# Performance work log

Hardware: AMD Instinct MI355X
Metric: run time of the kernel (lower is better)

## Reference

```python
import jax, jax.numpy as jnp
import numpy as np

B, S, L, D = 4, 8, 350, 768  # paragraphs, sentences/paragraph, padded pair length, hidden
P = B * S * (S - 1)          # number of ordered sentence pairs = 224

# pair p -> (z, j, k): same enumeration order as the torch nested loops
_IDX = np.array([(z, j, k) for z in range(B) for j in range(S) for k in range(S) if j != k])
# each pair contributes its first-sentence embedding to segment (z,j) and second to (z,k)
_SEG = np.stack([_IDX[:, 0] * S + _IDX[:, 1], _IDX[:, 0] * S + _IDX[:, 2]], axis=1).reshape(-1)  # [2P]


def setup_inputs() -> dict:
    key = jax.random.key(0)
    ks = jax.random.split(key, 8)
    sc = 0.02
    all_output = jax.random.normal(ks[0], (P, L, D), dtype=jnp.float32)
    first_sep = jax.random.randint(ks[1], (P,), 5, 150).astype(jnp.int32)           # > 1
    second_sep = (first_sep + jax.random.randint(ks[2], (P,), 5, 150)).astype(jnp.int32)  # > first_sep+1, < L
    W1 = jax.random.normal(ks[3], (D, D), dtype=jnp.float32) * sc
    b1 = jnp.zeros((D,), jnp.float32)
    v1 = jax.random.normal(ks[4], (D,), dtype=jnp.float32) * sc
    vb1 = jnp.zeros((), jnp.float32)
    W2 = jax.random.normal(ks[5], (D, D), dtype=jnp.float32) * sc
    b2 = jnp.zeros((D,), jnp.float32)
    v2 = jax.random.normal(ks[6], (D,), dtype=jnp.float32) * sc
    vb2 = jnp.zeros((), jnp.float32)
    return {"all_output": all_output, "first_sep": first_sep, "second_sep": second_sep,
            "W1": W1, "b1": b1, "v1": v1, "vb1": vb1,
            "W2": W2, "b2": b2, "v2": v2, "vb2": vb2}


def reference(all_output, first_sep, second_sep, W1, b1, v1, vb1, W2, b2, v2, vb2):
    # pair_embeddings = [CLS] token of every pair
    pair_embeddings = all_output[:, 0, :]  # [P, D]

    # ---- level one: masked attention pooling over word positions ----
    u = jnp.tanh(all_output @ W1 + b1)          # [P, L, D]
    scores = u @ v1 + vb1                       # [P, L]
    pos = jnp.arange(L)[None, :]                # [1, L]
    mask1 = (pos >= 1) & (pos < first_sep[:, None])                 # tokens 1..first_sep-1
    mask2 = (pos > first_sep[:, None]) & (pos < second_sep[:, None])  # first_sep+1..second_sep-1

    def pool(mask):
        s = jnp.where(mask, scores, -jnp.inf)
        w = jax.nn.softmax(s, axis=1)           # [P, L]
        return jnp.einsum('pl,pld->pd', w, all_output)

    e1 = pool(mask1)                            # [P, D] first-sentence embeddings
    e2 = pool(mask2)                            # [P, D] second-sentence embeddings
    emb = jnp.stack([e1, e2], axis=1).reshape(2 * P, D)  # [2P, D]

    # ---- level two: segment attention pooling per (paragraph, sentence) group ----
    seg = jnp.asarray(_SEG)                     # [2P] segment ids, num_segments = B*S
    u2 = jnp.tanh(emb @ W2 + b2)                # [2P, D]
    sc = u2 @ v2 + vb2                          # [2P]
    num_seg = B * S
    smax = jax.ops.segment_max(sc, seg, num_segments=num_seg)
    ex = jnp.exp(sc - smax[seg])
    denom = jax.ops.segment_sum(ex, seg, num_segments=num_seg)
    w = ex / denom[seg]                         # segment softmax weights
    out2 = jax.ops.segment_sum(w[:, None] * emb, seg, num_segments=num_seg).reshape(B, S, D)
    return (pair_embeddings, out2)
```

## Files before the change

kernel.cpp:

```cpp
#include <hip/hip_runtime.h>
#include <math.h>

#define LSEQ   350
#define DDIM   768
#define NPAIR  224
#define MROWS1 78400
#define NSLAB1 613
#define MAXSLAB 520
#define SPROWS 66688

typedef short bf16x8 __attribute__((ext_vector_type(8)));
typedef float f32x4  __attribute__((ext_vector_type(4)));

typedef const unsigned int __attribute__((address_space(1)))* gas_ptr;
typedef unsigned int __attribute__((address_space(3)))* las_ptr;

__device__ __forceinline__ void gload_lds16(const void* g, void* l) {
  __builtin_amdgcn_global_load_lds((gas_ptr)g, (las_ptr)l, 16, 0, 0);
}

__device__ __forceinline__ unsigned short f2bf(float x) {
  unsigned int u = __float_as_uint(x);
  unsigned int r = (u + 0x7FFFu + ((u >> 16) & 1u)) >> 16;
  return (unsigned short)r;
}

__device__ __forceinline__ float tanh_fast(float x) {
  float e = __expf(2.f * x);
  return 1.f - 2.f / (e + 1.f);
}

#define PREP_CV 2688
#define PREP_WT 1152
#define PREP_ZB 337
#define PREP_SCAN (PREP_CV + PREP_WT)
__global__ __launch_bounds__(256) void k_prep(
    const float* __restrict__ X, const float* __restrict__ W1,
    const float* __restrict__ W2, unsigned short* __restrict__ Wt1,
    unsigned short* __restrict__ Wt2, const int* __restrict__ ssep,
    int* __restrict__ off, unsigned int* __restrict__ zreg,
    unsigned short* __restrict__ Xbf) {
  const int b = blockIdx.x;
  const int t = threadIdx.x;
  if (b < PREP_CV) {
    const int p = b / 12;
    const int rem = b - p * 12;
    const int nrow = ssep[p] - 1;
    const int r0 = (rem >> 2) * 128 + (rem & 3) * 32;
    if (r0 >= nrow) return;
    const int lane = t & 63;
    int accv = 0;
    for (int i = lane; i < NPAIR; i += 64) accv += (i < p) ? (ssep[i] - 1) : 0;
#pragma unroll
    for (int d = 1; d < 64; d <<= 1) accv += __shfl_xor(accv, d);
    const int o = accv;
    if (t < 192) {
      const int half = t / 96;
      const int tt = t - half * 96;
      const int rmax = min(32, nrow - r0);
      const float* src = X + ((size_t)p * LSEQ + 1 + r0) * DDIM + tt * 8;
      unsigned short* dst = Xbf + (size_t)(o + r0) * DDIM + tt * 8;
#pragma unroll 4
      for (int rr = half; rr < rmax; rr += 2) {
        const float* s = src + (size_t)rr * DDIM;
        float4 x = *(const float4*)s;
        float4 y = *(const float4*)(s + 4);
        unsigned int ux = __float_as_uint(x.x) + 0x8000u;
        unsigned int uy = __float_as_uint(x.y) + 0x8000u;
        unsigned int uz = __float_as_uint(x.z) + 0x8000u;
        unsigned int uw = __float_as_uint(x.w) + 0x8000u;
        unsigned int vx = __float_as_uint(y.x) + 0x8000u;
        unsigned int vy = __float_as_uint(y.y) + 0x8000u;
        unsigned int vz = __float_as_uint(y.z) + 0x8000u;
        unsigned int vw = __float_as_uint(y.w) + 0x8000u;
        *(uint4*)(dst + (size_t)rr * DDIM) =
            make_uint4(__builtin_amdgcn_perm(uy, ux, 0x07060302u),
                       __builtin_amdgcn_perm(uw, uz, 0x07060302u),
                       __builtin_amdgcn_perm(vy, vx, 0x07060302u),
                       __builtin_amdgcn_perm(vw, vz, 0x07060302u));
      }
    }
  } else if (b < PREP_SCAN) {
    const int br = b - PREP_CV;
    const float* W = (br >= 576) ? W2 : W1;
    unsigned short* Wt = (br >= 576) ? Wt2 : Wt1;
    const int r = (br >= 576) ? br - 576 : br;
    const int bk = (r % 24) * 32, bn = (r / 24) * 32;
    __shared__ float tile[32][33];
    const int tx = t & 31, ty = t >> 5;
#pragma unroll
    for (int i = 0; i < 32; i += 8)
      tile[ty + i][tx] = W[(size_t)(bk + ty + i) * DDIM + bn + tx];
    __syncthreads();
#pragma unroll
    for (int i = 0; i < 32; i += 8)
      Wt[(size_t)(bn + ty + i) * DDIM + bk + tx] = f2bf(tile[tx][ty + i]);
  } else if (b == PREP_SCAN) {
    __shared__ int buf[256];
    int v = (t < NPAIR) ? (ssep[t] - 1) : 0;
    buf[t] = v;
    __syncthreads();
#pragma unroll
    for (int d = 1; d < 256; d <<= 1) {
      int add = (t >= d) ? buf[t - d] : 0;
      __syncthreads();
      buf[t] += add;
      __syncthreads();
    }
    if (t < NPAIR) off[t] = buf[t] - v;
    if (t == NPAIR - 1) off[NPAIR] = buf[t];
  } else {
    const int i = b - PREP_SCAN - 1;
    *((uint4*)zreg + (size_t)i * 256 + t) = make_uint4(0u, 0u, 0u, 0u);
  }
}

__global__ __launch_bounds__(256, 4) void k_gemm_c(
    const unsigned short* __restrict__ Xbf, const unsigned short* __restrict__ Wt,
    const float* __restrict__ bias, const float* __restrict__ vv,
    const int* __restrict__ off, float* __restrict__ scores_part) {
  const int Mtotal = off[NPAIR];
  const int b = blockIdx.x;
  const int g = b / 48, r = b - g * 48;
  const int slab = g * 8 + (r & 7);
  const int nchunk = r >> 3;
  if (slab * 128 >= Mtotal) return;

  const size_t arow0 = (size_t)slab * 128;
  const int n0 = nchunk * 128;

  __shared__ unsigned short As[2][128 * 32];
  __shared__ unsigned short Bs[2][128 * 32];

  const int t = threadIdx.x;
  const int lane = t & 63, w = t >> 6;
  const int l15 = t & 15;
  const int quad = (t >> 4) & 3;
  const int wm = w >> 1, wn = w & 1;
  const int lrow = lane >> 2;
  const int scol = ((lane & 3) ^ ((lane >> 3) & 3)) * 8;

  f32x4 acc[4][4];
#pragma unroll
  for (int mi = 0; mi < 4; ++mi)
#pragma unroll
    for (int ni = 0; ni < 4; ++ni)
#pragma unroll
      for (int q = 0; q < 4; ++q) acc[mi][ni][q] = 0.f;

  auto stage = [&](int bi, int kk0) {
#pragma unroll
    for (int j = 0; j < 2; ++j) {
      int seg = w * 2 + j;
      gload_lds16(Xbf + (arow0 + seg * 16 + lrow) * DDIM + kk0 + scol, &As[bi][seg * 512]);
      gload_lds16(Wt + (size_t)(n0 + seg * 16 + lrow) * DDIM + kk0 + scol, &Bs[bi][seg * 512]);
    }
  };

  stage(0, 0);
  __syncthreads();

  const int qs = (quad ^ ((l15 >> 1) & 3)) * 8;
  int cur = 0;
#pragma unroll 1
  for (int step = 0; step < DDIM / 32; ++step) {
    if (step < DDIM / 32 - 1) stage(cur ^ 1, (step + 1) * 32);

    bf16x8 a[4], bfr[4];
#pragma unroll
    for (int mi = 0; mi < 4; ++mi)
      a[mi] = *(const bf16x8*)&As[cur][(wm * 64 + mi * 16 + l15) * 32 + qs];
#pragma unroll
    for (int ni = 0; ni < 4; ++ni)
      bfr[ni] = *(const bf16x8*)&Bs[cur][(wn * 64 + ni * 16 + l15) * 32 + qs];
#pragma unroll
    for (int mi = 0; mi < 4; ++mi)
#pragma unroll
      for (int ni = 0; ni < 4; ++ni)
        acc[mi][ni] = __builtin_amdgcn_mfma_f32_16x16x32_bf16(a[mi], bfr[ni], acc[mi][ni], 0, 0, 0);
    __syncthreads();
    cur ^= 1;
  }

  float vvv[4], bbv[4];
#pragma unroll
  for (int ni = 0; ni < 4; ++ni) {
    int n = n0 + wn * 64 + ni * 16 + l15;
    vvv[ni] = vv[n];
    bbv[ni] = bias[n];
  }
  float* spdst = scores_part + (size_t)(nchunk * 2 + wn) * SPROWS;
#pragma unroll
  for (int mi = 0; mi < 4; ++mi) {
#pragma unroll
    for (int reg = 0; reg < 4; ++reg) {
      float s = 0.f;
#pragma unroll
      for (int ni = 0; ni < 4; ++ni)
        s += tanh_fast(acc[mi][ni][reg] + bbv[ni]) * vvv[ni];
      s += __shfl_xor(s, 1);
      s += __shfl_xor(s, 2);
      s += __shfl_xor(s, 4);
      s += __shfl_xor(s, 8);
      if (l15 == mi * 4 + reg) {
        int row = (int)arow0 + wm * 64 + mi * 16 + quad * 4 + reg;
        if (row < Mtotal) spdst[row] = s;
      }
    }
  }
}

__global__ __launch_bounds__(256, 2) void k_gemm_score(
    const float* __restrict__ X, const unsigned short* __restrict__ Wt,
    const float* __restrict__ bias, const float* __restrict__ vv,
    float* __restrict__ outs, int Mrows, int swz) {
  int slab, nchunk;
  if (swz) {
    int b = blockIdx.x;
    int g = b / 48, r = b - g * 48;
    slab = g * 8 + (r & 7);
    nchunk = r >> 3;
    if (slab >= NSLAB1) return;
  } else {
    slab = blockIdx.y;
    nchunk = blockIdx.x;
  }
  const int row0 = slab * 128;
  const int n0 = nchunk * 128;

  __shared__ unsigned short As[128][40];
  __shared__ unsigned short Bs[128][40];

  const int t = threadIdx.x;
  const int l15 = t & 15;
  const int quad = (t >> 4) & 3;
  const int w = t >> 6;
  const int wm = w >> 1, wn = w & 1;
  const int ar = t >> 3;
  const int ac = (t & 7) * 4;
  const int br = t >> 2;
  const int bc = (t & 3) * 8;

  f32x4 acc[4][4];
#pragma unroll
  for (int mi = 0; mi < 4; ++mi)
#pragma unroll
    for (int ni = 0; ni < 4; ++ni)
#pragma unroll
      for (int q = 0; q < 4; ++q) acc[mi][ni][q] = 0.f;

  for (int k0 = 0; k0 < DDIM; k0 += 32) {
#pragma unroll
    for (int pass = 0; pass < 4; ++pass) {
      int rr = ar + pass * 32;
      int row = row0 + rr;
      float4 x = make_float4(0.f, 0.f, 0.f, 0.f);
      if (row < Mrows) x = *(const float4*)(X + (size_t)row * DDIM + k0 + ac);
      unsigned int ux = __float_as_uint(x.x) + 0x8000u;
      unsigned int uy = __float_as_uint(x.y) + 0x8000u;
      unsigned int uz = __float_as_uint(x.z) + 0x8000u;
      unsigned int uw = __float_as_uint(x.w) + 0x8000u;
      *(uint2*)&As[rr][ac] = make_uint2(__builtin_amdgcn_perm(uy, ux, 0x07060302u),
                                        __builtin_amdgcn_perm(uw, uz, 0x07060302u));
    }
#pragma unroll
    for (int pp = 0; pp < 2; ++pp) {
      int rr = br + pp * 64;
      *(uint4*)&Bs[rr][bc] = *(const uint4*)(Wt + (size_t)(n0 + rr) * DDIM + k0 + bc);
    }
    __syncthreads();

    bf16x8 a[4], bfr[4];
#pragma unroll
    for (int mi = 0; mi < 4; ++mi)
      a[mi] = *(const bf16x8*)&As[wm * 64 + mi * 16 + l15][quad * 8];
#pragma unroll
    for (int ni = 0; ni < 4; ++ni)
      bfr[ni] = *(const bf16x8*)&Bs[wn * 64 + ni * 16 + l15][quad * 8];
#pragma unroll
    for (int mi = 0; mi < 4; ++mi)
#pragma unroll
      for (int ni = 0; ni < 4; ++ni)
        acc[mi][ni] = __builtin_amdgcn_mfma_f32_16x16x32_bf16(a[mi], bfr[ni], acc[mi][ni], 0, 0, 0);
    __syncthreads();
  }

  float vvv[4], bbv[4];
#pragma unroll
  for (int ni = 0; ni < 4; ++ni) {
    int n = n0 + wn * 64 + ni * 16 + l15;
    vvv[ni] = vv[n];
    bbv[ni] = bias[n];
  }
#pragma unroll
  for (int mi = 0; mi < 4; ++mi) {
#pragma unroll
    for (int reg = 0; reg < 4; ++reg) {
      float s = 0.f;
#pragma unroll
      for (int ni = 0; ni < 4; ++ni)
        s += tanh_fast(acc[mi][ni][reg] + bbv[ni]) * vvv[ni];
      s += __shfl_xor(s, 1);
      s += __shfl_xor(s, 2);
      s += __shfl_xor(s, 4);
      s += __shfl_xor(s, 8);
      if (l15 == mi * 4 + reg) {
        int row = row0 + wm * 64 + mi * 16 + quad * 4 + reg;
        if (row < Mrows) atomicAdd(&outs[row], s);
      }
    }
  }
}

__device__ __forceinline__ float block_reduce(float v, bool is_max, float* redbuf) {
#pragma unroll
  for (int off = 1; off < 64; off <<= 1) {
    float o = __shfl_xor(v, off);
    v = is_max ? fmaxf(v, o) : (v + o);
  }
  int wv = threadIdx.x >> 6;
  if ((threadIdx.x & 63) == 0) redbuf[wv] = v;
  __syncthreads();
  float r = is_max ? fmaxf(fmaxf(redbuf[0], redbuf[1]), fmaxf(redbuf[2], redbuf[3]))
                   : (redbuf[0] + redbuf[1] + redbuf[2] + redbuf[3]);
  __syncthreads();
  return r;
}

__global__ __launch_bounds__(256) void k_pool3(
    const unsigned short* __restrict__ Xbf, const float* __restrict__ X,
    const float* __restrict__ sp, const int* __restrict__ fsep,
    const int* __restrict__ ssep, const int* __restrict__ off,
    float* __restrict__ emb, float* __restrict__ out) {
  const int p = blockIdx.x, c = blockIdx.y, t = threadIdx.x;
  const int fs = fsep[p], ss = ssep[p];
  const int o = off[p];
  __shared__ float sw1[LSEQ], sw2[LSEQ];
  __shared__ float redbuf[4];

  float m1p = -INFINITY, m2p = -INFINITY;
  for (int l = t; l < LSEQ; l += 256) {
    float s = 0.f;
    if (l >= 1 && l < ss) {
      const int idx = o + l - 1;
#pragma unroll
      for (int c6 = 0; c6 < 12; ++c6) s += sp[(size_t)c6 * SPROWS + idx];
    }
    float s1 = (l >= 1 && l < fs) ? s : -INFINITY;
    float s2 = (l > fs && l < ss) ? s : -INFINITY;
    sw1[l] = s1; sw2[l] = s2;
    m1p = fmaxf(m1p, s1); m2p = fmaxf(m2p, s2);
  }
  __syncthreads();
  float m1 = block_reduce(m1p, true, redbuf);
  float m2 = block_reduce(m2p, true, redbuf);
  float d1p = 0.f, d2p = 0.f;
  for (int l = t; l < LSEQ; l += 256) {
    float e1v = __expf(sw1[l] - m1);
    float e2v = __expf(sw2[l] - m2);
    sw1[l] = e1v; sw2[l] = e2v;
    d1p += e1v; d2p += e2v;
  }
  __syncthreads();
  float inv1 = 1.f / block_reduce(d1p, false, redbuf);
  float inv2 = 1.f / block_reduce(d2p, false, redbuf);

  if (t < 192) {
    if (c == 0) {
      *(float4*)(out + (size_t)p * DDIM + t * 4) =
          *(const float4*)(X + (size_t)p * LSEQ * DDIM + t * 4);
    }

    const int nch = (ss + 2) >> 2;
    const int lo = 1 + c * nch;
    const int hi = min(ss, lo + nch);

    float A1[4] = {0.f, 0.f, 0.f, 0.f}, A2[4] = {0.f, 0.f, 0.f, 0.f};
    const unsigned short* xb = Xbf + (size_t)o * DDIM + t * 4;
#pragma unroll 4
    for (int l = lo; l < hi; ++l) {
      float wa = sw1[l] * inv1, wb = sw2[l] * inv2;
      uint2 xv = *(const uint2*)(xb + (size_t)(l - 1) * DDIM);
      float x0 = __uint_as_float((xv.x & 0xFFFFu) << 16);
      float x1 = __uint_as_float(xv.x & 0xFFFF0000u);
      float x2 = __uint_as_float((xv.y & 0xFFFFu) << 16);
      float x3 = __uint_as_float(xv.y & 0xFFFF0000u);
      A1[0] += wa * x0; A1[1] += wa * x1; A1[2] += wa * x2; A1[3] += wa * x3;
      A2[0] += wb * x0; A2[1] += wb * x1; A2[2] += wb * x2; A2[3] += wb * x3;
    }
    float* e1 = emb + (size_t)(2 * p) * DDIM + t * 4;
    float* e2 = emb + (size_t)(2 * p + 1) * DDIM + t * 4;
    atomicAdd(&e1[0], A1[0]); atomicAdd(&e1[1], A1[1]);
    atomicAdd(&e1[2], A1[2]); atomicAdd(&e1[3], A1[3]);
    atomicAdd(&e2[0], A2[0]); atomicAdd(&e2[1], A2[1]);
    atomicAdd(&e2[2], A2[2]); atomicAdd(&e2[3], A2[3]);
  }
}

__global__ __launch_bounds__(256) void k_w1t(const float* __restrict__ W,
                                             unsigned short* __restrict__ Wt) {
  __shared__ float tile[32][33];
  int bk = blockIdx.x * 32, bn = blockIdx.y * 32;
  int tx = threadIdx.x & 31, ty = threadIdx.x >> 5;
#pragma unroll
  for (int i = 0; i < 32; i += 8)
    tile[ty + i][tx] = W[(size_t)(bk + ty + i) * DDIM + bn + tx];
  __syncthreads();
#pragma unroll
  for (int i = 0; i < 32; i += 8)
    Wt[(size_t)(bn + ty + i) * DDIM + bk + tx] = f2bf(tile[tx][ty + i]);
}

__global__ __launch_bounds__(256) void k_pool(
    const float* __restrict__ X, const float* __restrict__ scores,
    const int* __restrict__ fsep, const int* __restrict__ ssep,
    float* __restrict__ emb, float* __restrict__ out) {
  const int p = blockIdx.x;
  const int c = blockIdx.y;
  const int t = threadIdx.x;
  const int fs = fsep[p], ss = ssep[p];
  __shared__ float sw1[LSEQ], sw2[LSEQ];
  __shared__ float redbuf[4];

  float m1p = -INFINITY, m2p = -INFINITY;
  for (int l = t; l < LSEQ; l += 256) {
    float s = scores[p * LSEQ + l];
    float s1 = (l >= 1 && l < fs) ? s : -INFINITY;
    float s2 = (l > fs && l < ss) ? s : -INFINITY;
    sw1[l] = s1; sw2[l] = s2;
    m1p = fmaxf(m1p, s1); m2p = fmaxf(m2p, s2);
  }
  __syncthreads();
  float m1 = block_reduce(m1p, true, redbuf);
  float m2 = block_reduce(m2p, true, redbuf);
  float d1p = 0.f, d2p = 0.f;
  for (int l = t; l < LSEQ; l += 256) {
    float e1v = __expf(sw1[l] - m1);
    float e2v = __expf(sw2[l] - m2);
    sw1[l] = e1v; sw2[l] = e2v;
    d1p += e1v; d2p += e2v;
  }
  __syncthreads();
  float inv1 = 1.f / block_reduce(d1p, false, redbuf);
  float inv2 = 1.f / block_reduce(d2p, false, redbuf);
  const float* base = X + (size_t)p * LSEQ * DDIM;
  if (c == 0) {
    float* po = out + (size_t)p * DDIM;
    po[t] = base[t]; po[t + 256] = base[t + 256]; po[t + 512] = base[t + 512];
  }
  if (t < 192) {
    float4 A1 = make_float4(0.f, 0.f, 0.f, 0.f);
    float4 A2 = make_float4(0.f, 0.f, 0.f, 0.f);
    for (int l = 1 + c; l < ss; l += 8) {
      float wa = sw1[l] * inv1, wb = sw2[l] * inv2;
      float4 x = *(const float4*)(base + (size_t)l * DDIM + 4 * t);
      A1.x += wa * x.x; A1.y += wa * x.y; A1.z += wa * x.z; A1.w += wa * x.w;
      A2.x += wb * x.x; A2.y += wb * x.y; A2.z += wb * x.z; A2.w += wb * x.w;
    }
    float* e1 = emb + (size_t)(2 * p) * DDIM + 4 * t;
    float* e2 = emb + (size_t)(2 * p + 1) * DDIM + 4 * t;
    atomicAdd(&e1[0], A1.x); atomicAdd(&e1[1], A1.y);
    atomicAdd(&e1[2], A1.z); atomicAdd(&e1[3], A1.w);
    atomicAdd(&e2[0], A2.x); atomicAdd(&e2[1], A2.y);
    atomicAdd(&e2[2], A2.z); atomicAdd(&e2[3], A2.w);
  }
}

__global__ __launch_bounds__(256) void k_segout(
    const float* __restrict__ emb, const float* __restrict__ sc,
    float* __restrict__ out2) {
  const int g = blockIdx.x;
  const int z = g >> 3, j = g & 7;
  const int t = threadIdx.x;
  int ee[14];
#pragma unroll
  for (int i = 0; i < 7; ++i) ee[i] = 2 * (z * 56 + j * 7 + i);
#pragma unroll
  for (int i = 0; i < 7; ++i) {
    int j2 = i + (i >= j ? 1 : 0);
    int kk = j - (j > j2 ? 1 : 0);
    ee[7 + i] = 2 * (z * 56 + j2 * 7 + kk) + 1;
  }
  float sv[14];
  float m = -INFINITY;
#pragma unroll
  for (int i = 0; i < 14; ++i) { sv[i] = sc[ee[i]]; m = fmaxf(m, sv[i]); }
  float den = 0.f;
#pragma unroll
  for (int i = 0; i < 14; ++i) { sv[i] = __expf(sv[i] - m); den += sv[i]; }
  float inv = 1.f / den;
  float a0 = 0.f, a1 = 0.f, a2 = 0.f;
#pragma unroll
  for (int i = 0; i < 14; ++i) {
    float wgt = sv[i] * inv;
    const float* er = emb + (size_t)ee[i] * DDIM;
    a0 += wgt * er[t]; a1 += wgt * er[t + 256]; a2 += wgt * er[t + 512];
  }
  out2[(size_t)g * DDIM + t] = a0;
  out2[(size_t)g * DDIM + t + 256] = a1;
  out2[(size_t)g * DDIM + t + 512] = a2;
}

extern "C" void kernel_launch(void* const* d_in, const int* in_sizes, int n_in,
                              void* d_out, int out_size, void* d_ws, size_t ws_size,
                              hipStream_t stream) {
  const float* X  = (const float*)d_in[0];
  const int* fs   = (const int*)d_in[1];
  const int* ss   = (const int*)d_in[2];
  const float* W1 = (const float*)d_in[3];
  const float* b1 = (const float*)d_in[4];
  const float* v1 = (const float*)d_in[5];
  const float* W2 = (const float*)d_in[7];
  const float* b2 = (const float*)d_in[8];
  const float* v2 = (const float*)d_in[9];
  float* out = (float*)d_out;

  char* ws = (char*)d_ws;
  const size_t XBF_ROWS = (size_t)MAXSLAB * 128 + 128;
  const size_t OFF_OFF  = XBF_ROWS * DDIM * 2;
  const size_t OFF_WT1  = OFF_OFF + 1024;
  const size_t OFF_WT2  = OFF_WT1 + 1179648;
  const size_t OFF_SP   = OFF_WT2 + 1179648;
  const size_t OFF_SC2  = OFF_SP + (size_t)12 * SPROWS * 4;
  const size_t OFF_EMB  = OFF_SC2 + 2048;
  const size_t ZBYTES   = (size_t)PREP_ZB * 4096;
  const size_t NEED     = OFF_SC2 + ZBYTES + 256;

  if (ws_size >= NEED) {
    unsigned short* Xbf = (unsigned short*)ws;
    int*   off     = (int*)(ws + OFF_OFF);
    unsigned short* Wt1 = (unsigned short*)(ws + OFF_WT1);
    unsigned short* Wt2 = (unsigned short*)(ws + OFF_WT2);
    float* spart    = (float*)(ws + OFF_SP);
    float* sc       = (float*)(ws + OFF_SC2);
    float* emb      = (float*)(ws + OFF_EMB);

    k_prep<<<PREP_SCAN + 1 + PREP_ZB, 256, 0, stream>>>(
        X, W1, W2, Wt1, Wt2, ss, off, (unsigned int*)sc, Xbf);
    k_gemm_c<<<65 * 48, 256, 0, stream>>>(Xbf, Wt1, b1, v1, off, spart);
    k_pool3<<<dim3(NPAIR, 4), 256, 0, stream>>>(Xbf, X, spart, fs, ss, off, emb, out);
    k_gemm_score<<<dim3(6, 4), 256, 0, stream>>>(emb, Wt2, b2, v2, sc, 448, 0);
    k_segout<<<32, 256, 0, stream>>>(emb, sc, out + (size_t)NPAIR * DDIM);
  } else {
    unsigned short* Wt = (unsigned short*)ws;
    float* scores = (float*)(ws + 1179648);
    float* emb    = (float*)(ws + 1493248);
    float* sc     = scores;

    k_w1t<<<dim3(24, 24), 256, 0, stream>>>(W1, Wt);
    hipMemsetAsync(scores, 0, MROWS1 * sizeof(float), stream);
    hipMemsetAsync(emb, 0, 448 * DDIM * sizeof(float), stream);
    k_gemm_score<<<77 * 48, 256, 0, stream>>>(X, Wt, b1, v1, scores, MROWS1, 1);
    k_pool<<<dim3(NPAIR, 8), 256, 0, stream>>>(X, scores, fs, ss, emb, out);
    k_w1t<<<dim3(24, 24), 256, 0, stream>>>(W2, Wt);
    hipMemsetAsync(sc, 0, 448 * sizeof(float), stream);
    k_gemm_score<<<dim3(6, 4), 256, 0, stream>>>(emb, Wt, b2, v2, sc, 448, 0);
    k_segout<<<32, 256, 0, stream>>>(emb, sc, out + (size_t)NPAIR * DDIM);
  }
}
```

Baseline: 468.2 us.

## Enlarge compacted GEMM tile to 256x256x64 with 512 threads and interleaved staging

```diff
diff --git a/kernel.cpp b/kernel.cpp
--- a/kernel.cpp
+++ b/kernel.cpp
@@ -7,6 +7,7 @@
 #define MROWS1 78400
 #define NSLAB1 613
 #define MAXSLAB 520
+#define MAXSLAB256 260
 #define SPROWS 66688
 
 typedef short bf16x8 __attribute__((ext_vector_type(8)));
@@ -115,71 +116,89 @@
   }
 }
 
-__global__ __launch_bounds__(256, 4) void k_gemm_c(
+__global__ __launch_bounds__(512, 2) void k_gemm_c(
     const unsigned short* __restrict__ Xbf, const unsigned short* __restrict__ Wt,
     const float* __restrict__ bias, const float* __restrict__ vv,
     const int* __restrict__ off, float* __restrict__ scores_part) {
   const int Mtotal = off[NPAIR];
   const int b = blockIdx.x;
-  const int g = b / 48, r = b - g * 48;
+  const int g = b / 24, r = b - g * 24;
   const int slab = g * 8 + (r & 7);
   const int nchunk = r >> 3;
-  if (slab * 128 >= Mtotal) return;
-
-  const size_t arow0 = (size_t)slab * 128;
-  const int n0 = nchunk * 128;
-
-  __shared__ unsigned short As[2][128 * 32];
-  __shared__ unsigned short Bs[2][128 * 32];
+  if (slab * 256 >= Mtotal) return;
+
+  const size_t arow0 = (size_t)slab * 256;
+  const int n0 = nchunk * 256;
+
+  __shared__ unsigned short As[2][256 * 64];
+  __shared__ unsigned short Bs[2][256 * 64];
 
   const int t = threadIdx.x;
   const int lane = t & 63, w = t >> 6;
   const int l15 = t & 15;
   const int quad = (t >> 4) & 3;
-  const int wm = w >> 1, wn = w & 1;
-  const int lrow = lane >> 2;
-  const int scol = ((lane & 3) ^ ((lane >> 3) & 3)) * 8;
-
-  f32x4 acc[4][4];
-#pragma unroll
-  for (int mi = 0; mi < 4; ++mi)
+  const int wm = w >> 2, wn = w & 3;
+  const int srow = (lane >> 3);
+  const int scol = ((lane & 7) ^ ((lane >> 3) & 7)) * 8;
+
+  f32x4 acc[8][4];
+#pragma unroll
+  for (int mi = 0; mi < 8; ++mi)
 #pragma unroll
     for (int ni = 0; ni < 4; ++ni)
 #pragma unroll
       for (int q = 0; q < 4; ++q) acc[mi][ni][q] = 0.f;
 
-  auto stage = [&](int bi, int kk0) {
+  auto stage_half = [&](int bi, int kt, int h) {
+    unsigned short* lb = (h < 2 ? &As[bi][0] : &Bs[bi][0]) + (h & 1) * 128 * 64;
+    const unsigned short* gb = (h < 2)
+        ? Xbf + (arow0 + (h & 1) * 128) * (size_t)DDIM
+        : Wt + (size_t)(n0 + (h & 1) * 128) * DDIM;
 #pragma unroll
     for (int j = 0; j < 2; ++j) {
-      int seg = w * 2 + j;
-      gload_lds16(Xbf + (arow0 + seg * 16 + lrow) * DDIM + kk0 + scol, &As[bi][seg * 512]);
-      gload_lds16(Wt + (size_t)(n0 + seg * 16 + lrow) * DDIM + kk0 + scol, &Bs[bi][seg * 512]);
+      int strip = w * 2 + j;
+      int rr = strip * 8 + srow;
+      gload_lds16(gb + (size_t)rr * DDIM + kt * 64 + scol, lb + strip * 512);
     }
   };
 
-  stage(0, 0);
-  __syncthreads();
-
-  const int qs = (quad ^ ((l15 >> 1) & 3)) * 8;
-  int cur = 0;
+  auto compute_tile = [&](int rb, int sb, int kts) {
+    bf16x8 a[4], bb[4];
+    const int sw = l15 & 7;
+#pragma unroll
+    for (int half = 0; half < 2; ++half) {
+#pragma unroll
+      for (int ni = 0; ni < 4; ++ni)
+        bb[ni] = *(const bf16x8*)&Bs[rb][(wn * 64 + ni * 16 + l15) * 64 +
+                                         (((half << 2) + quad) ^ sw) * 8];
+#pragma unroll
+      for (int mg = 0; mg < 2; ++mg) {
+#pragma unroll
+        for (int mi = 0; mi < 4; ++mi)
+          a[mi] = *(const bf16x8*)&As[rb][(wm * 128 + (mg * 4 + mi) * 16 + l15) * 64 +
+                                          (((half << 2) + quad) ^ sw) * 8];
+        if (kts >= 0) stage_half(sb, kts, half * 2 + mg);
+#pragma unroll
+        for (int mi = 0; mi < 4; ++mi)
+#pragma unroll
+          for (int ni = 0; ni < 4; ++ni)
+            acc[mg * 4 + mi][ni] = __builtin_amdgcn_mfma_f32_16x16x32_bf16(
+                a[mi], bb[ni], acc[mg * 4 + mi][ni], 0, 0, 0);
+      }
+    }
+  };
+
+#pragma unroll
+  for (int h = 0; h < 4; ++h) stage_half(0, 0, h);
+  __syncthreads();
+
 #pragma unroll 1
-  for (int step = 0; step < DDIM / 32; ++step) {
-    if (step < DDIM / 32 - 1) stage(cur ^ 1, (step + 1) * 32);
-
-    bf16x8 a[4], bfr[4];
-#pragma unroll
-    for (int mi = 0; mi < 4; ++mi)
-      a[mi] = *(const bf16x8*)&As[cur][(wm * 64 + mi * 16 + l15) * 32 + qs];
-#pragma unroll
-    for (int ni = 0; ni < 4; ++ni)
-      bfr[ni] = *(const bf16x8*)&Bs[cur][(wn * 64 + ni * 16 + l15) * 32 + qs];
-#pragma unroll
-    for (int mi = 0; mi < 4; ++mi)
-#pragma unroll
-      for (int ni = 0; ni < 4; ++ni)
-        acc[mi][ni] = __builtin_amdgcn_mfma_f32_16x16x32_bf16(a[mi], bfr[ni], acc[mi][ni], 0, 0, 0);
+  for (int iter = 0; iter < 6; ++iter) {
+    const int ktA = 2 * iter;
+    compute_tile(0, 1, ktA + 1);
     __syncthreads();
-    cur ^= 1;
+    compute_tile(1, 0, (ktA + 2 < 12) ? ktA + 2 : -1);
+    __syncthreads();
   }
 
   float vvv[4], bbv[4];
@@ -189,9 +208,9 @@
     vvv[ni] = vv[n];
     bbv[ni] = bias[n];
   }
-  float* spdst = scores_part + (size_t)(nchunk * 2 + wn) * SPROWS;
-#pragma unroll
-  for (int mi = 0; mi < 4; ++mi) {
+  float* spdst = scores_part + (size_t)(nchunk * 4 + wn) * SPROWS;
+#pragma unroll
+  for (int mi = 0; mi < 8; ++mi) {
 #pragma unroll
     for (int reg = 0; reg < 4; ++reg) {
       float s = 0.f;
@@ -202,8 +221,8 @@
       s += __shfl_xor(s, 2);
       s += __shfl_xor(s, 4);
       s += __shfl_xor(s, 8);
-      if (l15 == mi * 4 + reg) {
-        int row = (int)arow0 + wm * 64 + mi * 16 + quad * 4 + reg;
+      if (l15 == ((mi * 4 + reg) & 15)) {
+        int row = (int)arow0 + wm * 128 + mi * 16 + quad * 4 + reg;
         if (row < Mtotal) spdst[row] = s;
       }
     }
@@ -537,7 +556,7 @@
 
     k_prep<<<PREP_SCAN + 1 + PREP_ZB, 256, 0, stream>>>(
         X, W1, W2, Wt1, Wt2, ss, off, (unsigned int*)sc, Xbf);
-    k_gemm_c<<<65 * 48, 256, 0, stream>>>(Xbf, Wt1, b1, v1, off, spart);
+    k_gemm_c<<<(MAXSLAB256 / 8) * 24 + 24, 512, 0, stream>>>(Xbf, Wt1, b1, v1, off, spart);
     k_pool3<<<dim3(NPAIR, 4), 256, 0, stream>>>(Xbf, X, spart, fs, ss, off, emb, out);
     k_gemm_score<<<dim3(6, 4), 256, 0, stream>>>(emb, Wt2, b2, v2, sc, 448, 0);
     k_segout<<<32, 256, 0, stream>>>(emb, sc, out + (size_t)NPAIR * DDIM);
```

After: 473.8 us. Within noise of the previous version (+1.2%).
